# Performance work log

Hardware: AMD Instinct MI355X
Metric: run time of the kernel (lower is better)

The kernel has to match this reference:

```python
import jax, jax.numpy as jnp
import numpy as np

VOCAB, EMB, UNITS, B, T = 50000, 300, 256, 32, 512


def _lstm_scan(x, Wi, Wh, b, h0, c0):
    """Keras-order LSTM (gates i,f,c,o). x: [B,T,D]. Returns (outputs [B,T,U], h, c)."""
    xg = jnp.einsum('btd,dg->btg', x, Wi) + b  # precompute input projections [B,T,4U]

    def step(carry, xt):
        h, c = carry
        g = xt + h @ Wh
        i, f, gg, o = jnp.split(g, 4, axis=-1)
        c = jax.nn.sigmoid(f) * c + jax.nn.sigmoid(i) * jnp.tanh(gg)
        h = jax.nn.sigmoid(o) * jnp.tanh(c)
        return (h, c), h

    (h, c), hs = jax.lax.scan(step, (h0, c0), jnp.swapaxes(xg, 0, 1))
    return jnp.swapaxes(hs, 0, 1), h, c


def _bilstm(x, pf, pb, init=None):
    """Keras Bidirectional(LSTM(go_backwards=True), merge_mode='sum').
    'forward' sub-layer scans reversed input; 'backward' sub-layer scans original
    input and its output is time-reversed before summing."""
    Bsz = x.shape[0]
    if init is None:
        z = jnp.zeros((Bsz, UNITS), x.dtype)
        hf0, cf0, hb0, cb0 = z, z, z, z
    else:
        hf0, cf0, hb0, cb0 = init
    of, hf, cf = _lstm_scan(x[:, ::-1], *pf, hf0, cf0)
    ob, hb, cb = _lstm_scan(x, *pb, hb0, cb0)
    return of + ob[:, ::-1], hf, cf, hb, cb


def setup_inputs() -> dict:
    key = jax.random.key(0)
    ks = iter(jax.random.split(key, 32))
    d = {}
    d['x'] = jax.random.randint(next(ks), (B, T), 0, VOCAB, dtype=jnp.int32)
    d['emb'] = jax.random.normal(next(ks), (VOCAB, EMB), jnp.float32) * 0.05
    dims_in = [EMB, UNITS, UNITS]
    for l in (1, 2, 3):
        for dirc in ('f', 'b'):
            din = dims_in[l - 1]
            d[f'Wi{l}{dirc}'] = jax.random.normal(next(ks), (din, 4 * UNITS), jnp.float32) * 0.05
            d[f'Wh{l}{dirc}'] = jax.random.normal(next(ks), (UNITS, 4 * UNITS), jnp.float32) * 0.05
            d[f'b{l}{dirc}'] = jnp.zeros((4 * UNITS,), jnp.float32)
    return d


def reference(x, emb, Wi1f, Wh1f, b1f, Wi1b, Wh1b, b1b,
              Wi2f, Wh2f, b2f, Wi2b, Wh2b, b2b,
              Wi3f, Wh3f, b3f, Wi3b, Wh3b, b3b):
    h = emb[x]  # embedding lookup [B,T,EMB]
    h, hf, cf, hb, cb = _bilstm(h, (Wi1f, Wh1f, b1f), (Wi1b, Wh1b, b1b))
    h, hf, cf, hb, cb = _bilstm(h, (Wi2f, Wh2f, b2f), (Wi2b, Wh2b, b2b), (hf, cf, hb, cb))
    out, hf, cf, hb, cb = _bilstm(h, (Wi3f, Wh3f, b3f), (Wi3b, Wh3b, b3b), (hf, cf, hb, cb))
    return out, hf, cf, hb, cb
```

## Files before the change

kernel.cpp:

```cpp
#include <hip/hip_runtime.h>
#include <stdint.h>


typedef unsigned short u16;
typedef __bf16 bf16x8 __attribute__((ext_vector_type(8)));
typedef float f32x4 __attribute__((ext_vector_type(4)));

#define SCOPE_AGENT __HIP_MEMORY_SCOPE_AGENT

__device__ __forceinline__ float bf2f(u16 u) { return __uint_as_float(((unsigned)u) << 16); }
__device__ __forceinline__ u16 f2bf(float f) {
  unsigned u = __float_as_uint(f);
  unsigned r = (u + 0x7FFFu + ((u >> 16) & 1u)) >> 16;
  return (u16)r;
}
__device__ __forceinline__ float rdW(const void* p, size_t i, int isf) {
  return isf ? ((const float*)p)[i] : bf2f(((const u16*)p)[i]);
}
__device__ __forceinline__ float sigf(float x) { return 1.f / (1.f + __expf(-x)); }
__device__ __forceinline__ float tanh_(float x) { float e = __expf(2.f * x); return 1.f - 2.f / (e + 1.f); }

#define O_X0   0ull
#define O_WC1  10485760ull
#define O_WC2  11796480ull
#define O_WC3  12845056ull
#define O_WH   13893632ull
#define O_BIAS 17039360ull
#define O_FLAG 17063936ull
#define O_C0   17076352ull
#define O_CA   17141888ull
#define O_CB   17207424ull
#define O_CC   17272960ull
#define O_HSA  17338496ull
#define O_HSB  34148480ull
#define O_XG   50958464ull

#define HS_U16 16809984ull
#define HS_U4  1050624

__global__ void k_detect(const unsigned* __restrict__ embw, unsigned* flag) {
  int tid = threadIdx.x;
  unsigned w = embw[tid];
  unsigned e = (w >> 7) & 0xFFu;
  unsigned long long m = __ballot(e >= 100u && e < 128u);
  if (tid == 0) flag[0] = (__popcll(m) >= 32) ? 0u : 1u;
}

__global__ __launch_bounds__(256) void k_zero(uint4* __restrict__ p, int n) {
  uint4 z = {0u, 0u, 0u, 0u};
  for (int i = blockIdx.x * 256 + threadIdx.x; i < n; i += gridDim.x * 256) p[i] = z;
}

__global__ __launch_bounds__(256) void k_prep(
    const void* Wi1f, const void* Wi1b, const void* Wi2f, const void* Wi2b,
    const void* Wi3f, const void* Wi3b,
    const void* Wh1f, const void* Wh1b, const void* Wh2f, const void* Wh2b,
    const void* Wh3f, const void* Wh3b,
    const void* b1f, const void* b1b, const void* b2f, const void* b2b,
    const void* b3f, const void* b3b,
    const unsigned* __restrict__ flag,
    u16* Wc1, u16* Wc2, u16* Wc3, u16* WhC, float* bias, float* c0) {
  const int isf = (int)flag[0];
  int idx = blockIdx.x * 256 + threadIdx.x;
  if (idx < 2048 * 320) {
    int n = idx / 320, k = idx - n * 320;
    int dd = n >> 10, col = n & 1023;
    const void* W = dd ? Wi1b : Wi1f;
    Wc1[idx] = (k < 300) ? f2bf(rdW(W, (size_t)k * 1024 + col, isf)) : (u16)0;
  }
  if (idx < 2048 * 256) {
    int n = idx >> 8, k = idx & 255;
    int dd = n >> 10, col = n & 1023;
    Wc2[idx] = f2bf(rdW(dd ? Wi2b : Wi2f, (size_t)k * 1024 + col, isf));
    Wc3[idx] = f2bf(rdW(dd ? Wi3b : Wi3f, (size_t)k * 1024 + col, isf));
  }
  if (idx < 3 * 2048) {
    int l = idx >> 11, n = idx & 2047;
    int dd = n >> 10, col = n & 1023;
    const void* bp = (l == 0) ? (dd ? b1b : b1f) : (l == 1) ? (dd ? b2b : b2f) : (dd ? b3b : b3f);
    bias[idx] = rdW(bp, col, isf);
  }
  if (idx < 2 * 32 * 256) c0[idx] = 0.f;
  if (idx < 6 * 262144) {
    int mat = idx >> 18, pos = idx & 262143;
    const void* W = (mat == 0) ? Wh1f : (mat == 1) ? Wh1b : (mat == 2) ? Wh2f
                   : (mat == 3) ? Wh2b : (mat == 4) ? Wh3f : Wh3b;
    WhC[idx] = f2bf(rdW(W, (size_t)pos, isf));
  }
}

__global__ __launch_bounds__(256) void k_embed(const int* __restrict__ x,
                                               const void* __restrict__ emb,
                                               const unsigned* __restrict__ flag,
                                               u16* __restrict__ X0) {
  const int isf = (int)flag[0];
  int row = blockIdx.x;
  int t = row >> 5, b = row & 31;
  int tok = x[b * 512 + t];
  int tid = threadIdx.x;
  if (tid < 150) {
    unsigned pk;
    if (isf) {
      float2 v = *(const float2*)((const float*)emb + (size_t)tok * 300 + tid * 2);
      pk = (unsigned)f2bf(v.x) | ((unsigned)f2bf(v.y) << 16);
    } else {
      pk = *(const unsigned*)((const u16*)emb + (size_t)tok * 300 + tid * 2);
    }
    *(unsigned*)(X0 + (size_t)row * 320 + tid * 2) = pk;
  } else if (tid < 160) {
    *(unsigned*)(X0 + (size_t)row * 320 + 300 + (tid - 150) * 2) = 0u;
  }
}

__global__ __launch_bounds__(256) void k_gemm(const u16* __restrict__ A,
                                              const u16* __restrict__ Bt,
                                              const float* __restrict__ bias,
                                              u16* __restrict__ XG, int K) {
  __shared__ u16 As[128 * 32];
  __shared__ u16 Bs[128 * 32];
  const int tid = threadIdx.x;
  const int wv = tid >> 6, L = tid & 63, quad = L >> 4, l15 = L & 15;
  const int wm = wv & 1, wn = wv >> 1;
  const int bm = blockIdx.x & 127, bn = blockIdx.x >> 7;
  const u16* Ab = A + (size_t)(bm * 128) * K;
  const u16* Bb = Bt + (size_t)(bn * 128) * K;
  f32x4 z = {0.f, 0.f, 0.f, 0.f};
  f32x4 acc[4][4];
#pragma unroll
  for (int a = 0; a < 4; ++a)
#pragma unroll
    for (int b2 = 0; b2 < 4; ++b2) acc[a][b2] = z;
  const int srow = tid >> 2, sk = (tid & 3) * 8;
  for (int k0 = 0; k0 < K; k0 += 32) {
    __syncthreads();
    uint4 a0 = *(const uint4*)(Ab + (size_t)srow * K + k0 + sk);
    uint4 a1 = *(const uint4*)(Ab + (size_t)(srow + 64) * K + k0 + sk);
    uint4 b0 = *(const uint4*)(Bb + (size_t)srow * K + k0 + sk);
    uint4 b1 = *(const uint4*)(Bb + (size_t)(srow + 64) * K + k0 + sk);
    *(uint4*)&As[srow * 32 + sk] = a0;
    *(uint4*)&As[(srow + 64) * 32 + sk] = a1;
    *(uint4*)&Bs[srow * 32 + sk] = b0;
    *(uint4*)&Bs[(srow + 64) * 32 + sk] = b1;
    __syncthreads();
    bf16x8 af[4], bf[4];
#pragma unroll
    for (int t4 = 0; t4 < 4; ++t4) {
      af[t4] = *(const bf16x8*)&As[(wm * 64 + t4 * 16 + l15) * 32 + quad * 8];
      bf[t4] = *(const bf16x8*)&Bs[(wn * 64 + t4 * 16 + l15) * 32 + quad * 8];
    }
#pragma unroll
    for (int mt4 = 0; mt4 < 4; ++mt4)
#pragma unroll
      for (int nt4 = 0; nt4 < 4; ++nt4)
        acc[mt4][nt4] = __builtin_amdgcn_mfma_f32_16x16x32_bf16(af[mt4], bf[nt4], acc[mt4][nt4], 0, 0, 0);
  }
#pragma unroll
  for (int mt4 = 0; mt4 < 4; ++mt4)
#pragma unroll
    for (int nt4 = 0; nt4 < 4; ++nt4)
#pragma unroll
      for (int i = 0; i < 4; ++i) {
        int m = bm * 128 + wm * 64 + mt4 * 16 + quad * 4 + i;
        int n = bn * 128 + wn * 64 + nt4 * 16 + l15;
        XG[(size_t)m * 2048 + n] = f2bf(acc[mt4][nt4][i] + bias[n]);
      }
}

__global__ __launch_bounds__(512) void k_scan(const u16* __restrict__ XG,
                                              const u16* __restrict__ Whf,
                                              const u16* __restrict__ Whb,
                                              u16* hs, const u16* h0src,
                                              const float* __restrict__ c_src,
                                              float* __restrict__ c_dst) {
  const int wg = blockIdx.x;
  const int d = wg >> 3, r = wg & 7;
  const int tid = threadIdx.x;
  const int wv = tid >> 6, L = tid & 63, quad = L >> 4, l15 = L & 15;
  const int mt = wv & 1, p = wv >> 1;

  __shared__ u16 Ah[32][264];
  __shared__ float gbuf[32][132];

  const u16* Wh = d ? Whb : Whf;

  union U8 { u16 s[8]; bf16x8 v; };
  U8 bfrag[2][8];
#pragma unroll
  for (int t = 0; t < 2; ++t) {
    int nt = 2 * p + t;
    int col = (nt >> 1) * 256 + r * 32 + (nt & 1) * 16 + l15;
#pragma unroll
    for (int kt = 0; kt < 8; ++kt)
#pragma unroll
      for (int j = 0; j < 8; ++j)
        bfrag[t][kt].s[j] = Wh[(size_t)(kt * 32 + quad * 8 + j) * 1024 + col];
  }

  const int b_c = tid >> 4, j16 = tid & 15;
  const int gu = r * 32 + 2 * j16;
  float cv0 = c_src[(d * 32 + b_c) * 256 + gu];
  float cv1 = c_src[(d * 32 + b_c) * 256 + gu + 1];

  unsigned* hw = (unsigned*)hs;

  {
    unsigned hv[8];
    if (h0src) {
      const unsigned* h0w = (const unsigned*)h0src + (size_t)(d * 513 + 512) * 4096 + tid * 8;
#pragma unroll
      for (int q = 0; q < 8; ++q) hv[q] = h0w[q];
    } else {
#pragma unroll
      for (int q = 0; q < 8; ++q) hv[q] = 0x80008000u;
    }
    unsigned* dst = (unsigned*)&Ah[tid >> 4][(tid & 15) * 16];
#pragma unroll
    for (int q = 0; q < 8; ++q) dst[q] = hv[q] ^ 0x80008000u;
  }

  u16 xgr[2][4];
  {
    int tin = d ? 0 : 511;
#pragma unroll
    for (int t = 0; t < 2; ++t) {
      int nt = 2 * p + t;
      int col = d * 1024 + (nt >> 1) * 256 + r * 32 + (nt & 1) * 16 + l15;
      const u16* xp = XG + (size_t)(tin * 32 + mt * 16 + quad * 4) * 2048 + col;
#pragma unroll
      for (int i = 0; i < 4; ++i) xgr[t][i] = xp[(size_t)i * 2048];
    }
  }

  for (int s = 0; s < 512; ++s) {
    __syncthreads();

    f32x4 acc0 = {0.f, 0.f, 0.f, 0.f}, acc1 = {0.f, 0.f, 0.f, 0.f};
#pragma unroll
    for (int kt = 0; kt < 8; ++kt) {
      bf16x8 ah = *(const bf16x8*)&Ah[mt * 16 + l15][kt * 32 + quad * 8];
      acc0 = __builtin_amdgcn_mfma_f32_16x16x32_bf16(ah, bfrag[0][kt].v, acc0, 0, 0, 0);
      acc1 = __builtin_amdgcn_mfma_f32_16x16x32_bf16(ah, bfrag[1][kt].v, acc1, 0, 0, 0);
    }

#pragma unroll
    for (int i = 0; i < 4; ++i) {
      int bb = mt * 16 + quad * 4 + i;
      {
        int nt = 2 * p;
        gbuf[bb][(nt >> 1) * 32 + (nt & 1) * 16 + l15] = acc0[i] + bf2f(xgr[0][i]);
      }
      {
        int nt = 2 * p + 1;
        gbuf[bb][(nt >> 1) * 32 + (nt & 1) * 16 + l15] = acc1[i] + bf2f(xgr[1][i]);
      }
    }
    __syncthreads();

    {
      int lu = 2 * j16;
      float gi0 = gbuf[b_c][lu],      gi1 = gbuf[b_c][lu + 1];
      float gf0 = gbuf[b_c][32 + lu], gf1 = gbuf[b_c][32 + lu + 1];
      float gg0 = gbuf[b_c][64 + lu], gg1 = gbuf[b_c][64 + lu + 1];
      float go0 = gbuf[b_c][96 + lu], go1 = gbuf[b_c][96 + lu + 1];
      cv0 = sigf(gf0) * cv0 + sigf(gi0) * tanh_(gg0);
      cv1 = sigf(gf1) * cv1 + sigf(gi1) * tanh_(gg1);
      float h0f = sigf(go0) * tanh_(cv0);
      float h1f = sigf(go1) * tanh_(cv1);
      u16 e0 = f2bf(h0f); if (e0 == 0x8000u) e0 = 0;
      u16 e1 = f2bf(h1f); if (e1 == 0x8000u) e1 = 0;
      unsigned pk = ((unsigned)e0 | ((unsigned)e1 << 16)) ^ 0x80008000u;
      __hip_atomic_store(&hw[(size_t)(d * 513 + s + 1) * 4096 + b_c * 128 + r * 16 + j16],
                         pk, __ATOMIC_RELAXED, SCOPE_AGENT);
      if (s == 511) {
        c_dst[(d * 32 + b_c) * 256 + gu] = cv0;
        c_dst[(d * 32 + b_c) * 256 + gu + 1] = cv1;
      }
    }

    if (s < 511) {
      __syncthreads();

      {
        int tin = d ? (s + 1) : (510 - s);
#pragma unroll
        for (int t = 0; t < 2; ++t) {
          int nt = 2 * p + t;
          int col = d * 1024 + (nt >> 1) * 256 + r * 32 + (nt & 1) * 16 + l15;
          const u16* xp = XG + (size_t)(tin * 32 + mt * 16 + quad * 4) * 2048 + col;
#pragma unroll
          for (int i = 0; i < 4; ++i) xgr[t][i] = xp[(size_t)i * 2048];
        }
      }

      const unsigned long long* src =
          (const unsigned long long*)(hw + (size_t)(d * 513 + s + 1) * 4096) + tid * 4;
      unsigned long long w[4];
#pragma unroll
      for (int q2 = 0; q2 < 4; ++q2)
        w[q2] = __hip_atomic_load(src + q2, __ATOMIC_RELAXED, SCOPE_AGENT);
      for (;;) {
        bool all = true;
#pragma unroll
        for (int q2 = 0; q2 < 4; ++q2) {
          if ((unsigned)w[q2] == 0u || (unsigned)(w[q2] >> 32) == 0u) {
            all = false;
            w[q2] = __hip_atomic_load(src + q2, __ATOMIC_RELAXED, SCOPE_AGENT);
          }
        }
        if (all) break;
      }
      unsigned* dst = (unsigned*)&Ah[tid >> 4][(tid & 15) * 16];
#pragma unroll
      for (int q2 = 0; q2 < 4; ++q2) {
        dst[q2 * 2]     = ((unsigned)w[q2]) ^ 0x80008000u;
        dst[q2 * 2 + 1] = ((unsigned)(w[q2] >> 32)) ^ 0x80008000u;
      }
    }
  }
}

__global__ __launch_bounds__(256) void k_mkA(const u16* __restrict__ hs, u16* __restrict__ A23) {
  int row = blockIdx.x;
  int t = row >> 5, b = row & 31, u = threadIdx.x;
  float vf = bf2f(hs[(size_t)(t + 1) * 8192 + b * 256 + u] ^ 0x8000u);
  float vb = bf2f(hs[(size_t)(513 + 512 - t) * 8192 + b * 256 + u] ^ 0x8000u);
  A23[(size_t)row * 256 + u] = f2bf(vf + vb);
}

__global__ __launch_bounds__(256) void k_epi(const u16* __restrict__ hs,
                                             const float* __restrict__ cC,
                                             const unsigned* __restrict__ flag,
                                             void* __restrict__ outv) {
  const int isf = (int)flag[0];
  float* outf = (float*)outv;
  u16* outb = (u16*)outv;
  int u = threadIdx.x;
  if (blockIdx.x < 16384) {
    int b = blockIdx.x >> 9, s = blockIdx.x & 511;
    float v = bf2f(hs[(size_t)(s + 1) * 8192 + b * 256 + u] ^ 0x8000u) +
              bf2f(hs[(size_t)(513 + 512 - s) * 8192 + b * 256 + u] ^ 0x8000u);
    size_t o = (size_t)blockIdx.x * 256 + u;
    if (isf) outf[o] = v; else outb[o] = f2bf(v);
  } else {
    int j = blockIdx.x - 16384;
    const size_t base = 16384ull * 256;
    float vhf = bf2f(hs[(size_t)512 * 8192 + j * 256 + u] ^ 0x8000u);
    float vcf = cC[j * 256 + u];
    float vhb = bf2f(hs[(size_t)1025 * 8192 + j * 256 + u] ^ 0x8000u);
    float vcb = cC[(32 + j) * 256 + u];
    size_t o0 = base + (size_t)j * 256 + u;
    if (isf) {
      outf[o0] = vhf; outf[o0 + 8192] = vcf; outf[o0 + 16384] = vhb; outf[o0 + 24576] = vcb;
    } else {
      outb[o0] = f2bf(vhf); outb[o0 + 8192] = f2bf(vcf);
      outb[o0 + 16384] = f2bf(vhb); outb[o0 + 24576] = f2bf(vcb);
    }
  }
}

extern "C" void kernel_launch(void* const* d_in, const int* in_sizes, int n_in,
                              void* d_out, int out_size, void* d_ws, size_t ws_size,
                              hipStream_t stream) {
  (void)in_sizes; (void)n_in; (void)out_size; (void)ws_size;
  const int* x   = (const int*)d_in[0];
  const void* emb = d_in[1];
  const void* Wi1f = d_in[2];  const void* Wh1f = d_in[3];  const void* b1f = d_in[4];
  const void* Wi1b = d_in[5];  const void* Wh1b = d_in[6];  const void* b1b = d_in[7];
  const void* Wi2f = d_in[8];  const void* Wh2f = d_in[9];  const void* b2f = d_in[10];
  const void* Wi2b = d_in[11]; const void* Wh2b = d_in[12]; const void* b2b = d_in[13];
  const void* Wi3f = d_in[14]; const void* Wh3f = d_in[15]; const void* b3f = d_in[16];
  const void* Wi3b = d_in[17]; const void* Wh3b = d_in[18]; const void* b3b = d_in[19];

  char* ws = (char*)d_ws;
  u16* X0   = (u16*)(ws + O_X0);
  u16* A23  = (u16*)(ws + O_X0);
  u16* Wc1  = (u16*)(ws + O_WC1);
  u16* Wc2  = (u16*)(ws + O_WC2);
  u16* Wc3  = (u16*)(ws + O_WC3);
  u16* WhC  = (u16*)(ws + O_WH);
  float* bias = (float*)(ws + O_BIAS);
  unsigned* flag = (unsigned*)(ws + O_FLAG);
  float* c0 = (float*)(ws + O_C0);
  float* cA = (float*)(ws + O_CA);
  float* cB = (float*)(ws + O_CB);
  float* cC = (float*)(ws + O_CC);
  u16* hsA = (u16*)(ws + O_HSA);
  u16* hsB = (u16*)(ws + O_HSB);
  u16* XG  = (u16*)(ws + O_XG);

  k_detect<<<1, 64, 0, stream>>>((const unsigned*)emb, flag);
  k_prep<<<6144, 256, 0, stream>>>(Wi1f, Wi1b, Wi2f, Wi2b, Wi3f, Wi3b,
                                   Wh1f, Wh1b, Wh2f, Wh2b, Wh3f, Wh3b,
                                   b1f, b1b, b2f, b2b, b3f, b3b,
                                   flag, Wc1, Wc2, Wc3, WhC, bias, c0);
  k_zero<<<2048, 256, 0, stream>>>((uint4*)hsA, HS_U4);
  k_zero<<<2048, 256, 0, stream>>>((uint4*)hsB, HS_U4);
  k_embed<<<16384, 256, 0, stream>>>(x, emb, flag, X0);

  k_gemm<<<2048, 256, 0, stream>>>(X0, Wc1, bias + 0, XG, 320);
  k_scan<<<16, 512, 0, stream>>>(XG, WhC + 0 * 262144, WhC + 1 * 262144, hsA, nullptr, c0, cA);
  k_mkA<<<16384, 256, 0, stream>>>(hsA, A23);
  k_gemm<<<2048, 256, 0, stream>>>(A23, Wc2, bias + 2048, XG, 256);
  k_scan<<<16, 512, 0, stream>>>(XG, WhC + 2 * 262144, WhC + 3 * 262144, hsB, hsA, cA, cB);
  k_zero<<<2048, 256, 0, stream>>>((uint4*)hsA, HS_U4);
  k_mkA<<<16384, 256, 0, stream>>>(hsB, A23);
  k_gemm<<<2048, 256, 0, stream>>>(A23, Wc3, bias + 4096, XG, 256);
  k_scan<<<16, 512, 0, stream>>>(XG, WhC + 4 * 262144, WhC + 5 * 262144, hsA, hsB, cB, cC);

  k_epi<<<16416, 256, 0, stream>>>(hsA, cC, flag, d_out);
}
```

Before: 4.014 ms.

## Split LSTM recurrence over 4 workgroups per direction instead of 8

The recurrent scan now uses 4 workgroups per direction, each owning 64 hidden units, in place of 8 workgroups of 32 units. Each wave holds four MFMA B-fragment tiles and each thread computes four cells. A workgroup writes its own h slice straight into LDS and polls global memory only for the other three slices. One barrier per step is removed. The aim is to cut cross-workgroup synchronization and global polling traffic on the latency-bound sequential path, at the price of more per-workgroup MFMA and activation work and higher register pressure.

```diff
diff --git a/kernel.cpp b/kernel.cpp
--- a/kernel.cpp
+++ b/kernel.cpp
@@ -35,7 +35,6 @@
 #define O_HSB  34148480ull
 #define O_XG   50958464ull
 
-#define HS_U16 16809984ull
 #define HS_U4  1050624
 
 __global__ void k_detect(const unsigned* __restrict__ embw, unsigned* flag) {
@@ -166,29 +165,29 @@
       }
 }
 
-__global__ __launch_bounds__(512) void k_scan(const u16* __restrict__ XG,
-                                              const u16* __restrict__ Whf,
-                                              const u16* __restrict__ Whb,
-                                              u16* hs, const u16* h0src,
-                                              const float* __restrict__ c_src,
-                                              float* __restrict__ c_dst) {
+__global__ __launch_bounds__(512, 2) void k_scan(const u16* __restrict__ XG,
+                                                 const u16* __restrict__ Whf,
+                                                 const u16* __restrict__ Whb,
+                                                 u16* hs, const u16* h0src,
+                                                 const float* __restrict__ c_src,
+                                                 float* __restrict__ c_dst) {
   const int wg = blockIdx.x;
-  const int d = wg >> 3, r = wg & 7;
+  const int d = wg >> 2, q = wg & 3;
   const int tid = threadIdx.x;
   const int wv = tid >> 6, L = tid & 63, quad = L >> 4, l15 = L & 15;
-  const int mt = wv & 1, p = wv >> 1;
+  const int mt = wv & 1, ng = wv >> 1;
 
   __shared__ u16 Ah[32][264];
-  __shared__ float gbuf[32][132];
+  __shared__ float gbuf[32][257];
 
   const u16* Wh = d ? Whb : Whf;
 
   union U8 { u16 s[8]; bf16x8 v; };
-  U8 bfrag[2][8];
-#pragma unroll
-  for (int t = 0; t < 2; ++t) {
-    int nt = 2 * p + t;
-    int col = (nt >> 1) * 256 + r * 32 + (nt & 1) * 16 + l15;
+  U8 bfrag[4][8];
+#pragma unroll
+  for (int t = 0; t < 4; ++t) {
+    int ci = (ng * 4 + t) * 16 + l15;
+    int col = (ci >> 6) * 256 + q * 64 + (ci & 63);
 #pragma unroll
     for (int kt = 0; kt < 8; ++kt)
 #pragma unroll
@@ -196,35 +195,35 @@
         bfrag[t][kt].s[j] = Wh[(size_t)(kt * 32 + quad * 8 + j) * 1024 + col];
   }
 
-  const int b_c = tid >> 4, j16 = tid & 15;
-  const int gu = r * 32 + 2 * j16;
-  float cv0 = c_src[(d * 32 + b_c) * 256 + gu];
-  float cv1 = c_src[(d * 32 + b_c) * 256 + gu + 1];
+  const int b_c = tid >> 4, j = tid & 15;
+  float cv[4];
+#pragma unroll
+  for (int e = 0; e < 4; ++e)
+    cv[e] = c_src[(d * 32 + b_c) * 256 + q * 64 + 4 * j + e];
 
   unsigned* hw = (unsigned*)hs;
 
   {
-    unsigned hv[8];
+    int hb = tid >> 4, pair0 = (tid & 15) * 8;
     if (h0src) {
-      const unsigned* h0w = (const unsigned*)h0src + (size_t)(d * 513 + 512) * 4096 + tid * 8;
-#pragma unroll
-      for (int q = 0; q < 8; ++q) hv[q] = h0w[q];
+      const unsigned* h0w = (const unsigned*)h0src + ((size_t)(d * 513 + 512) * 32 + hb) * 128 + pair0;
+#pragma unroll
+      for (int k = 0; k < 8; ++k)
+        *(unsigned*)&Ah[hb][(pair0 + k) * 2] = h0w[k] ^ 0x80008000u;
     } else {
 #pragma unroll
-      for (int q = 0; q < 8; ++q) hv[q] = 0x80008000u;
-    }
-    unsigned* dst = (unsigned*)&Ah[tid >> 4][(tid & 15) * 16];
-#pragma unroll
-    for (int q = 0; q < 8; ++q) dst[q] = hv[q] ^ 0x80008000u;
-  }
-
-  u16 xgr[2][4];
+      for (int k = 0; k < 8; ++k)
+        *(unsigned*)&Ah[hb][(pair0 + k) * 2] = 0u;
+    }
+  }
+
+  u16 xgr[4][4];
   {
     int tin = d ? 0 : 511;
 #pragma unroll
-    for (int t = 0; t < 2; ++t) {
-      int nt = 2 * p + t;
-      int col = d * 1024 + (nt >> 1) * 256 + r * 32 + (nt & 1) * 16 + l15;
+    for (int t = 0; t < 4; ++t) {
+      int ci = (ng * 4 + t) * 16 + l15;
+      int col = d * 1024 + (ci >> 6) * 256 + q * 64 + (ci & 63);
       const u16* xp = XG + (size_t)(tin * 32 + mt * 16 + quad * 4) * 2048 + col;
 #pragma unroll
       for (int i = 0; i < 4; ++i) xgr[t][i] = xp[(size_t)i * 2048];
@@ -234,86 +233,95 @@
   for (int s = 0; s < 512; ++s) {
     __syncthreads();
 
-    f32x4 acc0 = {0.f, 0.f, 0.f, 0.f}, acc1 = {0.f, 0.f, 0.f, 0.f};
+    f32x4 acc[4] = {{0.f, 0.f, 0.f, 0.f}, {0.f, 0.f, 0.f, 0.f},
+                    {0.f, 0.f, 0.f, 0.f}, {0.f, 0.f, 0.f, 0.f}};
 #pragma unroll
     for (int kt = 0; kt < 8; ++kt) {
       bf16x8 ah = *(const bf16x8*)&Ah[mt * 16 + l15][kt * 32 + quad * 8];
-      acc0 = __builtin_amdgcn_mfma_f32_16x16x32_bf16(ah, bfrag[0][kt].v, acc0, 0, 0, 0);
-      acc1 = __builtin_amdgcn_mfma_f32_16x16x32_bf16(ah, bfrag[1][kt].v, acc1, 0, 0, 0);
-    }
-
-#pragma unroll
-    for (int i = 0; i < 4; ++i) {
-      int bb = mt * 16 + quad * 4 + i;
-      {
-        int nt = 2 * p;
-        gbuf[bb][(nt >> 1) * 32 + (nt & 1) * 16 + l15] = acc0[i] + bf2f(xgr[0][i]);
-      }
-      {
-        int nt = 2 * p + 1;
-        gbuf[bb][(nt >> 1) * 32 + (nt & 1) * 16 + l15] = acc1[i] + bf2f(xgr[1][i]);
-      }
+#pragma unroll
+      for (int t = 0; t < 4; ++t)
+        acc[t] = __builtin_amdgcn_mfma_f32_16x16x32_bf16(ah, bfrag[t][kt].v, acc[t], 0, 0, 0);
+    }
+
+#pragma unroll
+    for (int t = 0; t < 4; ++t) {
+      int ci = (ng * 4 + t) * 16 + l15;
+#pragma unroll
+      for (int i = 0; i < 4; ++i)
+        gbuf[mt * 16 + quad * 4 + i][ci] = acc[t][i] + bf2f(xgr[t][i]);
     }
     __syncthreads();
 
     {
-      int lu = 2 * j16;
-      float gi0 = gbuf[b_c][lu],      gi1 = gbuf[b_c][lu + 1];
-      float gf0 = gbuf[b_c][32 + lu], gf1 = gbuf[b_c][32 + lu + 1];
-      float gg0 = gbuf[b_c][64 + lu], gg1 = gbuf[b_c][64 + lu + 1];
-      float go0 = gbuf[b_c][96 + lu], go1 = gbuf[b_c][96 + lu + 1];
-      cv0 = sigf(gf0) * cv0 + sigf(gi0) * tanh_(gg0);
-      cv1 = sigf(gf1) * cv1 + sigf(gi1) * tanh_(gg1);
-      float h0f = sigf(go0) * tanh_(cv0);
-      float h1f = sigf(go1) * tanh_(cv1);
-      u16 e0 = f2bf(h0f); if (e0 == 0x8000u) e0 = 0;
-      u16 e1 = f2bf(h1f); if (e1 == 0x8000u) e1 = 0;
-      unsigned pk = ((unsigned)e0 | ((unsigned)e1 << 16)) ^ 0x80008000u;
-      __hip_atomic_store(&hw[(size_t)(d * 513 + s + 1) * 4096 + b_c * 128 + r * 16 + j16],
-                         pk, __ATOMIC_RELAXED, SCOPE_AGENT);
+      u16 eh[4];
+#pragma unroll
+      for (int e = 0; e < 4; ++e) {
+        int lu = 4 * j + e;
+        float gi = gbuf[b_c][lu];
+        float gf = gbuf[b_c][64 + lu];
+        float gg = gbuf[b_c][128 + lu];
+        float go = gbuf[b_c][192 + lu];
+        cv[e] = sigf(gf) * cv[e] + sigf(gi) * tanh_(gg);
+        float h = sigf(go) * tanh_(cv[e]);
+        u16 ev = f2bf(h); if (ev == 0x8000u) ev = 0;
+        eh[e] = ev;
+      }
+      unsigned pk0 = ((unsigned)eh[0] | ((unsigned)eh[1] << 16)) ^ 0x80008000u;
+      unsigned pk1 = ((unsigned)eh[2] | ((unsigned)eh[3] << 16)) ^ 0x80008000u;
+      size_t base = ((size_t)(d * 513 + s + 1) * 32 + b_c) * 128 + q * 32 + 2 * j;
+      __hip_atomic_store(&hw[base],     pk0, __ATOMIC_RELAXED, SCOPE_AGENT);
+      __hip_atomic_store(&hw[base + 1], pk1, __ATOMIC_RELAXED, SCOPE_AGENT);
+      *(unsigned*)&Ah[b_c][q * 64 + 4 * j]     = pk0 ^ 0x80008000u;
+      *(unsigned*)&Ah[b_c][q * 64 + 4 * j + 2] = pk1 ^ 0x80008000u;
       if (s == 511) {
-        c_dst[(d * 32 + b_c) * 256 + gu] = cv0;
-        c_dst[(d * 32 + b_c) * 256 + gu + 1] = cv1;
+#pragma unroll
+        for (int e = 0; e < 4; ++e)
+          c_dst[(d * 32 + b_c) * 256 + q * 64 + 4 * j + e] = cv[e];
       }
     }
 
     if (s < 511) {
-      __syncthreads();
-
       {
         int tin = d ? (s + 1) : (510 - s);
 #pragma unroll
-        for (int t = 0; t < 2; ++t) {
-          int nt = 2 * p + t;
-          int col = d * 1024 + (nt >> 1) * 256 + r * 32 + (nt & 1) * 16 + l15;
+        for (int t = 0; t < 4; ++t) {
+          int ci = (ng * 4 + t) * 16 + l15;
+          int col = d * 1024 + (ci >> 6) * 256 + q * 64 + (ci & 63);
           const u16* xp = XG + (size_t)(tin * 32 + mt * 16 + quad * 4) * 2048 + col;
 #pragma unroll
           for (int i = 0; i < 4; ++i) xgr[t][i] = xp[(size_t)i * 2048];
         }
       }
 
-      const unsigned long long* src =
-          (const unsigned long long*)(hw + (size_t)(d * 513 + s + 1) * 4096) + tid * 4;
-      unsigned long long w[4];
-#pragma unroll
-      for (int q2 = 0; q2 < 4; ++q2)
-        w[q2] = __hip_atomic_load(src + q2, __ATOMIC_RELAXED, SCOPE_AGENT);
+      size_t sb = (size_t)(d * 513 + s + 2) * 32;
+      sb = ((size_t)(d * 513 + s + 1) * 32 + b_c) * 128;
+      unsigned v[6];
+      size_t pidx[6];
+#pragma unroll
+      for (int pp = 0; pp < 3; ++pp) {
+        int q2 = (q + 1 + pp) & 3;
+        pidx[pp * 2]     = sb + q2 * 32 + 2 * j;
+        pidx[pp * 2 + 1] = sb + q2 * 32 + 2 * j + 1;
+      }
+#pragma unroll
+      for (int p2 = 0; p2 < 6; ++p2)
+        v[p2] = __hip_atomic_load(&hw[pidx[p2]], __ATOMIC_RELAXED, SCOPE_AGENT);
       for (;;) {
         bool all = true;
 #pragma unroll
-        for (int q2 = 0; q2 < 4; ++q2) {
-          if ((unsigned)w[q2] == 0u || (unsigned)(w[q2] >> 32) == 0u) {
+        for (int p2 = 0; p2 < 6; ++p2) {
+          if (v[p2] == 0u) {
             all = false;
-            w[q2] = __hip_atomic_load(src + q2, __ATOMIC_RELAXED, SCOPE_AGENT);
+            v[p2] = __hip_atomic_load(&hw[pidx[p2]], __ATOMIC_RELAXED, SCOPE_AGENT);
           }
         }
         if (all) break;
       }
-      unsigned* dst = (unsigned*)&Ah[tid >> 4][(tid & 15) * 16];
-#pragma unroll
-      for (int q2 = 0; q2 < 4; ++q2) {
-        dst[q2 * 2]     = ((unsigned)w[q2]) ^ 0x80008000u;
-        dst[q2 * 2 + 1] = ((unsigned)(w[q2] >> 32)) ^ 0x80008000u;
+#pragma unroll
+      for (int pp = 0; pp < 3; ++pp) {
+        int q2 = (q + 1 + pp) & 3;
+        *(unsigned*)&Ah[b_c][q2 * 64 + 4 * j]     = v[pp * 2]     ^ 0x80008000u;
+        *(unsigned*)&Ah[b_c][q2 * 64 + 4 * j + 2] = v[pp * 2 + 1] ^ 0x80008000u;
       }
     }
   }
@@ -342,13 +350,13 @@
     size_t o = (size_t)blockIdx.x * 256 + u;
     if (isf) outf[o] = v; else outb[o] = f2bf(v);
   } else {
-    int j = blockIdx.x - 16384;
+    int jj = blockIdx.x - 16384;
     const size_t base = 16384ull * 256;
-    float vhf = bf2f(hs[(size_t)512 * 8192 + j * 256 + u] ^ 0x8000u);
-    float vcf = cC[j * 256 + u];
-    float vhb = bf2f(hs[(size_t)1025 * 8192 + j * 256 + u] ^ 0x8000u);
-    float vcb = cC[(32 + j) * 256 + u];
-    size_t o0 = base + (size_t)j * 256 + u;
+    float vhf = bf2f(hs[(size_t)512 * 8192 + jj * 256 + u] ^ 0x8000u);
+    float vcf = cC[jj * 256 + u];
+    float vhb = bf2f(hs[(size_t)1025 * 8192 + jj * 256 + u] ^ 0x8000u);
+    float vcb = cC[(32 + jj) * 256 + u];
+    size_t o0 = base + (size_t)jj * 256 + u;
     if (isf) {
       outf[o0] = vhf; outf[o0 + 8192] = vcf; outf[o0 + 16384] = vhb; outf[o0 + 24576] = vcb;
     } else {
@@ -398,14 +406,14 @@
   k_embed<<<16384, 256, 0, stream>>>(x, emb, flag, X0);
 
   k_gemm<<<2048, 256, 0, stream>>>(X0, Wc1, bias + 0, XG, 320);
-  k_scan<<<16, 512, 0, stream>>>(XG, WhC + 0 * 262144, WhC + 1 * 262144, hsA, nullptr, c0, cA);
+  k_scan<<<8, 512, 0, stream>>>(XG, WhC + 0 * 262144, WhC + 1 * 262144, hsA, nullptr, c0, cA);
   k_mkA<<<16384, 256, 0, stream>>>(hsA, A23);
   k_gemm<<<2048, 256, 0, stream>>>(A23, Wc2, bias + 2048, XG, 256);
-  k_scan<<<16, 512, 0, stream>>>(XG, WhC + 2 * 262144, WhC + 3 * 262144, hsB, hsA, cA, cB);
+  k_scan<<<8, 512, 0, stream>>>(XG, WhC + 2 * 262144, WhC + 3 * 262144, hsB, hsA, cA, cB);
   k_zero<<<2048, 256, 0, stream>>>((uint4*)hsA, HS_U4);
   k_mkA<<<16384, 256, 0, stream>>>(hsB, A23);
   k_gemm<<<2048, 256, 0, stream>>>(A23, Wc3, bias + 4096, XG, 256);
-  k_scan<<<16, 512, 0, stream>>>(XG, WhC + 4 * 262144, WhC + 5 * 262144, hsA, hsB, cB, cC);
+  k_scan<<<8, 512, 0, stream>>>(XG, WhC + 4 * 262144, WhC + 5 * 262144, hsA, hsB, cB, cC);
 
   k_epi<<<16416, 256, 0, stream>>>(hsA, cC, flag, d_out);
 }
```

Result: slower. 4.935 ms (+22.9%).
